# Performance work log

Measured on AMD Instinct MI355X. Metric: run time of the kernel, lower is better.

## Reference

```python
import jax, jax.numpy as jnp
from jax import lax
import numpy as np

B, N = 2, 261888          # images per GPU, total anchors (1024px FPN)
PRE_NMS = 6000            # config.PRE_NMS_LIMIT
PROPOSAL_COUNT = 1000     # proposal_count
NMS_THR = 0.7             # nms_threshold
STD = jnp.array([0.1, 0.1, 0.2, 0.2], jnp.float32)  # RPN_BBOX_STD_DEV


def setup_inputs() -> dict:
    key = jax.random.key(0)
    k1, k2, k3, k4 = jax.random.split(key, 4)
    rpn_class = jax.random.uniform(k1, (B, N, 2), dtype=jnp.float32)
    rpn_bbox = jax.random.normal(k2, (B, N, 4), dtype=jnp.float32)
    # valid normalized anchors: y1x1 in [0,0.9], h/w in [0.01,0.11]
    yx1 = jax.random.uniform(k3, (B, N, 2), dtype=jnp.float32) * 0.9
    hw = jax.random.uniform(k4, (B, N, 2), dtype=jnp.float32) * 0.1 + 0.01
    anchors = jnp.concatenate([yx1, yx1 + hw], axis=-1)
    return {"rpn_class": rpn_class, "rpn_bbox": rpn_bbox, "anchors": anchors}


def apply_box_deltas(boxes, deltas):
    h = boxes[..., 2] - boxes[..., 0]
    w = boxes[..., 3] - boxes[..., 1]
    cy = boxes[..., 0] + 0.5 * h + deltas[..., 0] * h
    cx = boxes[..., 1] + 0.5 * w + deltas[..., 1] * w
    h = h * jnp.exp(deltas[..., 2])
    w = w * jnp.exp(deltas[..., 3])
    y1 = cy - 0.5 * h
    x1 = cx - 0.5 * w
    return jnp.stack([y1, x1, y1 + h, x1 + w], axis=-1)


def pairwise_iou(b):  # b: [K,4] (y1,x1,y2,x2)
    y1, x1, y2, x2 = b[:, 0], b[:, 1], b[:, 2], b[:, 3]
    area = (y2 - y1) * (x2 - x1)
    ih = jnp.maximum(jnp.minimum(y2[:, None], y2[None, :]) - jnp.maximum(y1[:, None], y1[None, :]), 0.0)
    iw = jnp.maximum(jnp.minimum(x2[:, None], x2[None, :]) - jnp.maximum(x1[:, None], x1[None, :]), 0.0)
    inter = ih * iw
    return inter / (area[:, None] + area[None, :] - inter + 1e-8)


def nms_single(boxes, scores):
    # boxes [K,4] already sorted by descending score (top_k sorted=True)
    K = boxes.shape[0]
    iou = pairwise_iou(boxes)  # [K,K]

    def step(keep, xs):
        i, row = xs
        kept = jnp.logical_not(jnp.any(keep & (row > NMS_THR)))
        return keep.at[i].set(kept), None

    keep, _ = lax.scan(step, jnp.zeros((K,), jnp.bool_), (jnp.arange(K), iou))
    masked = jnp.where(keep, scores, -jnp.inf)
    _, idx = lax.top_k(masked, PROPOSAL_COUNT)
    props = boxes[idx]                      # [P,4]
    valid = keep[idx][:, None]              # pad with zeros like tf NMS padding
    return jnp.where(valid, props, 0.0)


def reference(rpn_class, rpn_bbox, anchors):
    scores = rpn_class[:, :, 1]                       # [B,N]
    deltas = rpn_bbox * STD.reshape(1, 1, 4)          # [B,N,4]
    k = min(PRE_NMS, anchors.shape[1])
    _, ix = lax.top_k(scores, k)                      # [B,k] sorted desc
    scores_k = jnp.take_along_axis(scores, ix, axis=1)
    deltas_k = jnp.take_along_axis(deltas, ix[..., None], axis=1)
    anchors_k = jnp.take_along_axis(anchors, ix[..., None], axis=1)
    boxes = apply_box_deltas(anchors_k, deltas_k)
    boxes = jnp.clip(boxes, 0.0, 1.0)                 # window [0,0,1,1]
    return jax.vmap(nms_single)(boxes, scores_k)      # [B,PROPOSAL_COUNT,4]
```

## Files before the change

kernel.cpp:

```cpp
#include <hip/hip_runtime.h>
#include <cstdint>

#define BATCH   2
#define NANCH   261888
#define PRE_NMS 6000
#define PROP    1000
#define SEG_CAP 8192
#define ECAP    65536
#define NT      94
#define RG      2
#define NMS_THR 0.7f
#define FLOOR   63488
#define WIN     2048
#define CAND_CAP 16384

typedef unsigned long long u64;
typedef unsigned int u32;

#define META_OFF   0u
#define BOXES_OFF  256u
#define EDGES_OFF  262400u
#define HIST_OFF   786688u
#define RANK_OFF   803072u
#define SEG_OFF    819456u
#define CAND_OFF   950528u
#define ZERO_N     (2u * WIN)

__global__ void k_zero(u32* p, int n, int* meta) {
    int i = blockIdx.x * blockDim.x + threadIdx.x;
    if (i < n) p[i] = 0u;
    if (i < 8) meta[i] = 0;
}

__device__ __forceinline__ int score_bucket(float s) {
    int bk = (int)(s * 65536.0f);
    return bk < 0 ? 0 : (bk > 65535 ? 65535 : bk);
}

__global__ __launch_bounds__(256) void k_histcand(const float2* __restrict__ cls2,
                                                  int* __restrict__ hist,
                                                  int* __restrict__ meta,
                                                  u64* __restrict__ cand) {
    __shared__ u64 lbuf[512];
    __shared__ u32 lcnt;
    __shared__ int lbase;
    int b = blockIdx.y, t = threadIdx.x;
    if (t == 0) lcnt = 0;
    __syncthreads();
    int* ccnt = meta + 2;
    for (int i = blockIdx.x * 256 + t; i < NANCH; i += 256 * 256) {
        float s = cls2[(size_t)b * NANCH + i].y;
        int bk = score_bucket(s);
        if (bk >= FLOOR) {
            atomicAdd(&hist[b * WIN + (bk - FLOOR)], 1);
            u64 key = ((u64)__float_as_uint(s) << 32) | (u32)(~(u32)i);
            u32 lp = atomicAdd(&lcnt, 1u);
            if (lp < 512) lbuf[lp] = key;
            else {
                int gp = atomicAdd(&ccnt[b], 1);
                if (gp < CAND_CAP) cand[b * CAND_CAP + gp] = key;
            }
        }
    }
    __syncthreads();
    int n = lcnt < 512u ? (int)lcnt : 512;
    if (t == 0) lbase = n ? atomicAdd(&ccnt[b], n) : 0;
    __syncthreads();
    for (int k = t; k < n; k += 256) {
        int gp = lbase + k;
        if (gp < CAND_CAP) cand[b * CAND_CAP + gp] = lbuf[k];
    }
}

__global__ __launch_bounds__(256) void k_ranks(const int* __restrict__ hist,
                                               int* __restrict__ rank_start,
                                               int* __restrict__ meta) {
    __shared__ int s[256];
    int b = blockIdx.x, t = threadIdx.x;
    const int* h = hist + b * WIN;
    int base = t * 8;
    int hv[8];
    int sum = 0;
    for (int c = 0; c < 8; ++c) { hv[c] = h[base + c]; sum += hv[c]; }
    s[t] = sum;
    __syncthreads();
    for (int off = 1; off < 256; off <<= 1) {
        int add = (t + off < 256) ? s[t + off] : 0;
        __syncthreads();
        s[t] += add;
        __syncthreads();
    }
    int above = (t + 1 < 256) ? s[t + 1] : 0;
    int acc = 0;
    int* rs = rank_start + b * WIN;
    for (int c = 7; c >= 0; --c) {
        int r = above + acc;
        rs[base + c] = r;
        acc += hv[c];
        if (r < PRE_NMS && r + hv[c] >= PRE_NMS) meta[b] = FLOOR + base + c;
    }
    if (t == 0 && s[0] < PRE_NMS) meta[b] = FLOOR;
}

__global__ __launch_bounds__(256) void k_scatterbuild(const u64* __restrict__ cand,
                                                      const int* __restrict__ meta,
                                                      int* __restrict__ rank,
                                                      u64* __restrict__ seg,
                                                      const float4* __restrict__ anchors,
                                                      const float4* __restrict__ bbox,
                                                      float4* __restrict__ boxes) {
    #pragma clang fp contract(off)
    int b = blockIdx.y;
    int thr = meta[b];
    int cc = meta[2 + b]; if (cc > CAND_CAP) cc = CAND_CAP;
    int idx = blockIdx.x * 256 + threadIdx.x;
    if (idx >= cc) return;
    u64 key = cand[b * CAND_CAP + idx];
    float s = __uint_as_float((u32)(key >> 32));
    int bk = score_bucket(s);
    if (bk < thr) return;
    int slot = atomicAdd(&rank[b * WIN + (bk - FLOOR)], 1);
    if (slot >= SEG_CAP) return;
    seg[(b << 13) + slot] = key;
    u32 ai = ~(u32)(key & 0xffffffffull);
    float4 a = anchors[(size_t)b * NANCH + ai];
    float4 d = bbox[(size_t)b * NANCH + ai];
    float dy = d.x * 0.1f, dx = d.y * 0.1f, dh = d.z * 0.2f, dw = d.w * 0.2f;
    float h = a.z - a.x;
    float w = a.w - a.y;
    float cy = a.x + 0.5f * h + dy * h;
    float cx = a.y + 0.5f * w + dx * w;
    h = h * expf(dh);
    w = w * expf(dw);
    float y1 = cy - 0.5f * h;
    float x1 = cx - 0.5f * w;
    float y2 = y1 + h;
    float x2 = x1 + w;
    y1 = fminf(fmaxf(y1, 0.f), 1.f);
    x1 = fminf(fmaxf(x1, 0.f), 1.f);
    y2 = fminf(fmaxf(y2, 0.f), 1.f);
    x2 = fminf(fmaxf(x2, 0.f), 1.f);
    boxes[(b << 13) + slot] = make_float4(y1, x1, y2, x2);
}

__global__ __launch_bounds__(256) void k_bsort(const int* __restrict__ meta,
                                               const int* __restrict__ rank,
                                               u64* __restrict__ seg,
                                               float4* __restrict__ boxes) {
    int b = blockIdx.y;
    int bkw = blockIdx.x * 256 + threadIdx.x;
    if (FLOOR + bkw < meta[b]) return;
    int en = rank[b * WIN + bkw]; if (en > SEG_CAP) en = SEG_CAP;
    int st = (bkw + 1 < WIN) ? rank[b * WIN + bkw + 1] : 0;
    if (st >= en - 1) return;
    u64* sg = seg + (b << 13);
    float4* bx = boxes + (b << 13);
    for (int i = st; i < en - 1; ++i) {
        u64 best = sg[i]; int bi = i;
        for (int j = i + 1; j < en; ++j) {
            u64 v = sg[j];
            if (v > best) { best = v; bi = j; }
        }
        if (bi != i) {
            sg[bi] = sg[i]; sg[i] = best;
            float4 tmp = bx[bi]; bx[bi] = bx[i]; bx[i] = tmp;
        }
    }
}

__global__ __launch_bounds__(256) void k_mask(const float4* __restrict__ boxes,
                                              u32* __restrict__ edges, int* __restrict__ ecnt) {
    #pragma clang fp contract(off)
    __shared__ float4 tb[64];
    __shared__ float ta69[64];
    int gx = blockIdx.x, T = blockIdx.y, b = blockIdx.z;
    if (gx * 8 + 7 < T) return;
    int wv = threadIdx.x >> 6, lane = threadIdx.x & 63;
    if (threadIdx.x < 64) {
        int c = T * 64 + threadIdx.x;
        float4 v = (c < PRE_NMS) ? boxes[(b << 13) + c] : make_float4(0.f, 0.f, 0.f, 0.f);
        tb[threadIdx.x] = v;
        ta69[threadIdx.x] = 0.69f * ((v.z - v.x) * (v.w - v.y));
    }
    __syncthreads();
    int W0 = gx * 8 + wv * RG;
    if (W0 + RG - 1 < T) return;
    float4 rb[RG]; float a69[RG]; float area_r[RG]; int jg[RG];
    #pragma unroll
    for (int r = 0; r < RG; ++r) {
        int W = W0 + r;
        int j = W * 64 + lane;
        bool ok = (W < NT) && (j < PRE_NMS);
        float4 v = ok ? boxes[(b << 13) + j] : make_float4(0.f, 0.f, 0.f, 0.f);
        rb[r] = v;
        float ar = (v.z - v.x) * (v.w - v.y);
        area_r[r] = ar;
        a69[r] = 0.69f * ar;
        jg[r] = j;
    }
    for (int c = 0; c < 64; ++c) {
        float4 bi = tb[c];
        float t69 = ta69[c];
        int ig = T * 64 + c;
        #pragma unroll
        for (int r = 0; r < RG; ++r) {
            float ih = fminf(bi.z, rb[r].z) - fmaxf(bi.x, rb[r].x); ih = fmaxf(ih, 0.f);
            float iw = fminf(bi.w, rb[r].w) - fmaxf(bi.y, rb[r].y); iw = fmaxf(iw, 0.f);
            float inter = ih * iw;
            if (inter > fmaxf(t69, a69[r])) {
                float ai = (bi.z - bi.x) * (bi.w - bi.y);
                float iou = inter / (ai + area_r[r] - inter + 1e-8f);
                if (iou > NMS_THR && ig < jg[r]) {
                    int pos = atomicAdd(&ecnt[b], 1);
                    if (pos < ECAP) edges[(b << 16) + pos] = ((u32)jg[r] << 13) | (u32)ig;
                }
            }
        }
    }
}

__global__ __launch_bounds__(512) void k_resolveout(const u32* __restrict__ edges,
                                                    const int* __restrict__ ecnt,
                                                    const float4* __restrict__ boxes,
                                                    float* __restrict__ out) {
    __shared__ unsigned char st[6016];
    __shared__ u32 cnt[6016];
    __shared__ u64 kw[NT];
    __shared__ int wp[NT + 1];
    __shared__ int changed;
    int b = blockIdx.x, t = threadIdx.x;
    int E = ecnt[b]; if (E > ECAP) E = ECAP;
    const u32* eb = edges + ((size_t)b << 16);
    for (int i = t; i < PROP * 4; i += 512) out[b * PROP * 4 + i] = 0.f;
    for (int j = t; j < 6016; j += 512) st[j] = 1;
    __syncthreads();
    for (int k = t; k < E; k += 512) st[eb[k] >> 13] = 0;
    __syncthreads();
    while (true) {
        if (t == 0) changed = 0;
        __syncthreads();
        for (int k = t; k < E; k += 512) {
            u32 e = eb[k]; int i = e & 8191, j = e >> 13;
            if (st[i] == 1 && st[j] == 0) { st[j] = 2; changed = 1; }
        }
        __syncthreads();
        for (int j = t; j < 6016; j += 512) cnt[j] = 0;
        __syncthreads();
        for (int k = t; k < E; k += 512) {
            u32 e = eb[k]; int i = e & 8191, j = e >> 13;
            if (st[i] != 2) atomicAdd(&cnt[j], 1u);
        }
        __syncthreads();
        for (int j = t; j < 6016; j += 512) {
            if (st[j] == 0 && cnt[j] == 0) { st[j] = 1; changed = 1; }
        }
        __syncthreads();
        if (!changed) break;
    }
    if (t < NT) {
        int base = t * 64;
        int lim = PRE_NMS - base; if (lim > 64) lim = 64;
        u64 bits = 0;
        for (int l = 0; l < lim; ++l) if (st[base + l] == 1) bits |= (1ull << l);
        kw[t] = bits;
        wp[t + 1] = __popcll(bits);
    }
    if (t == 0) wp[0] = 0;
    __syncthreads();
    if (t == 0) { for (int i = 1; i <= NT; ++i) wp[i] += wp[i - 1]; }
    __syncthreads();
    float4* out4 = (float4*)(out + b * PROP * 4);
    for (int j = t; j < PRE_NMS; j += 512) {
        u64 w = kw[j >> 6];
        int bit = j & 63;
        if ((w >> bit) & 1ull) {
            int rank = wp[j >> 6] + __popcll(w & ((1ull << bit) - 1ull));
            if (rank < PROP) out4[rank] = boxes[(b << 13) + j];
        }
    }
}

extern "C" void kernel_launch(void* const* d_in, const int* in_sizes, int n_in,
                              void* d_out, int out_size, void* d_ws, size_t ws_size,
                              hipStream_t stream) {
    const float2* cls2    = (const float2*)d_in[0];
    const float4* bbox    = (const float4*)d_in[1];
    const float4* anchors = (const float4*)d_in[2];
    float* out = (float*)d_out;
    char* w = (char*)d_ws;
    int*    meta   = (int*)(w + META_OFF);
    float4* boxes  = (float4*)(w + BOXES_OFF);
    u32*    edges  = (u32*)(w + EDGES_OFF);
    int*    hist   = (int*)(w + HIST_OFF);
    int*    rank   = (int*)(w + RANK_OFF);
    u64*    seg    = (u64*)(w + SEG_OFF);
    u64*    cand   = (u64*)(w + CAND_OFF);

    k_zero<<<dim3((ZERO_N + 255) / 256), 256, 0, stream>>>((u32*)hist, ZERO_N, meta);
    k_histcand<<<dim3(256, BATCH), 256, 0, stream>>>(cls2, hist, meta, cand);
    k_ranks<<<dim3(BATCH), 256, 0, stream>>>(hist, rank, meta);
    k_scatterbuild<<<dim3(CAND_CAP / 256, BATCH), 256, 0, stream>>>(cand, meta, rank, seg,
                                                                    anchors, bbox, boxes);
    k_bsort<<<dim3(WIN / 256, BATCH), 256, 0, stream>>>(meta, rank, seg, boxes);
    k_mask<<<dim3((NT + 7) / 8, NT, BATCH), 256, 0, stream>>>(boxes, edges, meta + 4);
    k_resolveout<<<dim3(BATCH), 512, 0, stream>>>(edges, meta + 4, boxes, out);
}
```

Measured before the change: 129.9 us.

## Drop zero kernel and global histogram atomics; use per-block candidate segments

Removes the k_zero launch and the global histogram atomics. Each histcand block now writes its candidates to its own fixed segment along with a count, and k_ranks rebuilds the histogram in shared memory from those segments. The scatter kernel reads per-block segments with 64 threads, and the prefix sum in resolveout becomes a parallel scan instead of a serial loop. The trade-off is that k_ranks does the histogram serially in only two blocks, and candidates beyond 1024 per block are dropped.

New measurement: 125.7 us. -3.2%, faster.

```diff
diff --git a/kernel.cpp b/kernel.cpp
--- a/kernel.cpp
+++ b/kernel.cpp
@@ -12,7 +12,7 @@
 #define NMS_THR 0.7f
 #define FLOOR   63488
 #define WIN     2048
-#define CAND_CAP 16384
+#define BSEG    1024
 
 typedef unsigned long long u64;
 typedef unsigned int u32;
@@ -20,17 +20,10 @@
 #define META_OFF   0u
 #define BOXES_OFF  256u
 #define EDGES_OFF  262400u
-#define HIST_OFF   786688u
-#define RANK_OFF   803072u
-#define SEG_OFF    819456u
-#define CAND_OFF   950528u
-#define ZERO_N     (2u * WIN)
-
-__global__ void k_zero(u32* p, int n, int* meta) {
-    int i = blockIdx.x * blockDim.x + threadIdx.x;
-    if (i < n) p[i] = 0u;
-    if (i < 8) meta[i] = 0;
-}
+#define RANK_OFF   786688u
+#define SEG_OFF    803072u
+#define BCNT_OFF   934144u
+#define CAND_OFF   936192u
 
 __device__ __forceinline__ int score_bucket(float s) {
     int bk = (int)(s * 65536.0f);
@@ -38,50 +31,49 @@
 }
 
 __global__ __launch_bounds__(256) void k_histcand(const float2* __restrict__ cls2,
-                                                  int* __restrict__ hist,
-                                                  int* __restrict__ meta,
+                                                  int* __restrict__ bcnt,
                                                   u64* __restrict__ cand) {
-    __shared__ u64 lbuf[512];
+    __shared__ u64 lbuf[BSEG];
     __shared__ u32 lcnt;
-    __shared__ int lbase;
-    int b = blockIdx.y, t = threadIdx.x;
+    int b = blockIdx.y, blk = blockIdx.x, t = threadIdx.x;
     if (t == 0) lcnt = 0;
     __syncthreads();
-    int* ccnt = meta + 2;
-    for (int i = blockIdx.x * 256 + t; i < NANCH; i += 256 * 256) {
+    for (int i = blk * 256 + t; i < NANCH; i += 256 * 256) {
         float s = cls2[(size_t)b * NANCH + i].y;
         int bk = score_bucket(s);
         if (bk >= FLOOR) {
-            atomicAdd(&hist[b * WIN + (bk - FLOOR)], 1);
             u64 key = ((u64)__float_as_uint(s) << 32) | (u32)(~(u32)i);
             u32 lp = atomicAdd(&lcnt, 1u);
-            if (lp < 512) lbuf[lp] = key;
-            else {
-                int gp = atomicAdd(&ccnt[b], 1);
-                if (gp < CAND_CAP) cand[b * CAND_CAP + gp] = key;
-            }
-        }
-    }
-    __syncthreads();
-    int n = lcnt < 512u ? (int)lcnt : 512;
-    if (t == 0) lbase = n ? atomicAdd(&ccnt[b], n) : 0;
-    __syncthreads();
-    for (int k = t; k < n; k += 256) {
-        int gp = lbase + k;
-        if (gp < CAND_CAP) cand[b * CAND_CAP + gp] = lbuf[k];
-    }
-}
-
-__global__ __launch_bounds__(256) void k_ranks(const int* __restrict__ hist,
+            if (lp < BSEG) lbuf[lp] = key;
+        }
+    }
+    __syncthreads();
+    int n = lcnt < (u32)BSEG ? (int)lcnt : BSEG;
+    if (t == 0) bcnt[b * 256 + blk] = n;
+    u64* dst = cand + ((size_t)(b * 256 + blk) << 10);
+    for (int k = t; k < n; k += 256) dst[k] = lbuf[k];
+}
+
+__global__ __launch_bounds__(256) void k_ranks(const int* __restrict__ bcnt,
+                                               const u64* __restrict__ cand,
                                                int* __restrict__ rank_start,
                                                int* __restrict__ meta) {
+    __shared__ int hist[WIN];
     __shared__ int s[256];
     int b = blockIdx.x, t = threadIdx.x;
-    const int* h = hist + b * WIN;
+    for (int c = t; c < WIN; c += 256) hist[c] = 0;
+    __syncthreads();
+    int cnt = bcnt[b * 256 + t];
+    const u64* src = cand + ((size_t)(b * 256 + t) << 10);
+    for (int k = 0; k < cnt; ++k) {
+        float sc = __uint_as_float((u32)(src[k] >> 32));
+        atomicAdd(&hist[score_bucket(sc) - FLOOR], 1);
+    }
+    __syncthreads();
     int base = t * 8;
     int hv[8];
     int sum = 0;
-    for (int c = 0; c < 8; ++c) { hv[c] = h[base + c]; sum += hv[c]; }
+    for (int c = 0; c < 8; ++c) { hv[c] = hist[base + c]; sum += hv[c]; }
     s[t] = sum;
     __syncthreads();
     for (int off = 1; off < 256; off <<= 1) {
@@ -99,48 +91,53 @@
         acc += hv[c];
         if (r < PRE_NMS && r + hv[c] >= PRE_NMS) meta[b] = FLOOR + base + c;
     }
-    if (t == 0 && s[0] < PRE_NMS) meta[b] = FLOOR;
-}
-
-__global__ __launch_bounds__(256) void k_scatterbuild(const u64* __restrict__ cand,
-                                                      const int* __restrict__ meta,
-                                                      int* __restrict__ rank,
-                                                      u64* __restrict__ seg,
-                                                      const float4* __restrict__ anchors,
-                                                      const float4* __restrict__ bbox,
-                                                      float4* __restrict__ boxes) {
+    if (t == 0) {
+        meta[4 + b] = 0;
+        if (s[0] < PRE_NMS) meta[b] = FLOOR;
+    }
+}
+
+__global__ __launch_bounds__(64) void k_scatterbuild(const u64* __restrict__ cand,
+                                                     const int* __restrict__ bcnt,
+                                                     const int* __restrict__ meta,
+                                                     int* __restrict__ rank,
+                                                     u64* __restrict__ seg,
+                                                     const float4* __restrict__ anchors,
+                                                     const float4* __restrict__ bbox,
+                                                     float4* __restrict__ boxes) {
     #pragma clang fp contract(off)
-    int b = blockIdx.y;
+    int b = blockIdx.y, blk = blockIdx.x;
     int thr = meta[b];
-    int cc = meta[2 + b]; if (cc > CAND_CAP) cc = CAND_CAP;
-    int idx = blockIdx.x * 256 + threadIdx.x;
-    if (idx >= cc) return;
-    u64 key = cand[b * CAND_CAP + idx];
-    float s = __uint_as_float((u32)(key >> 32));
-    int bk = score_bucket(s);
-    if (bk < thr) return;
-    int slot = atomicAdd(&rank[b * WIN + (bk - FLOOR)], 1);
-    if (slot >= SEG_CAP) return;
-    seg[(b << 13) + slot] = key;
-    u32 ai = ~(u32)(key & 0xffffffffull);
-    float4 a = anchors[(size_t)b * NANCH + ai];
-    float4 d = bbox[(size_t)b * NANCH + ai];
-    float dy = d.x * 0.1f, dx = d.y * 0.1f, dh = d.z * 0.2f, dw = d.w * 0.2f;
-    float h = a.z - a.x;
-    float w = a.w - a.y;
-    float cy = a.x + 0.5f * h + dy * h;
-    float cx = a.y + 0.5f * w + dx * w;
-    h = h * expf(dh);
-    w = w * expf(dw);
-    float y1 = cy - 0.5f * h;
-    float x1 = cx - 0.5f * w;
-    float y2 = y1 + h;
-    float x2 = x1 + w;
-    y1 = fminf(fmaxf(y1, 0.f), 1.f);
-    x1 = fminf(fmaxf(x1, 0.f), 1.f);
-    y2 = fminf(fmaxf(y2, 0.f), 1.f);
-    x2 = fminf(fmaxf(x2, 0.f), 1.f);
-    boxes[(b << 13) + slot] = make_float4(y1, x1, y2, x2);
+    int cc = bcnt[b * 256 + blk];
+    const u64* src = cand + ((size_t)(b * 256 + blk) << 10);
+    for (int idx = threadIdx.x; idx < cc; idx += 64) {
+        u64 key = src[idx];
+        float s = __uint_as_float((u32)(key >> 32));
+        int bk = score_bucket(s);
+        if (bk < thr) continue;
+        int slot = atomicAdd(&rank[b * WIN + (bk - FLOOR)], 1);
+        if (slot >= SEG_CAP) continue;
+        seg[(b << 13) + slot] = key;
+        u32 ai = ~(u32)(key & 0xffffffffull);
+        float4 a = anchors[(size_t)b * NANCH + ai];
+        float4 d = bbox[(size_t)b * NANCH + ai];
+        float dy = d.x * 0.1f, dx = d.y * 0.1f, dh = d.z * 0.2f, dw = d.w * 0.2f;
+        float h = a.z - a.x;
+        float w = a.w - a.y;
+        float cy = a.x + 0.5f * h + dy * h;
+        float cx = a.y + 0.5f * w + dx * w;
+        h = h * expf(dh);
+        w = w * expf(dw);
+        float y1 = cy - 0.5f * h;
+        float x1 = cx - 0.5f * w;
+        float y2 = y1 + h;
+        float x2 = x1 + w;
+        y1 = fminf(fmaxf(y1, 0.f), 1.f);
+        x1 = fminf(fmaxf(x1, 0.f), 1.f);
+        y2 = fminf(fmaxf(y2, 0.f), 1.f);
+        x2 = fminf(fmaxf(x2, 0.f), 1.f);
+        boxes[(b << 13) + slot] = make_float4(y1, x1, y2, x2);
+    }
 }
 
 __global__ __launch_bounds__(256) void k_bsort(const int* __restrict__ meta,
@@ -267,8 +264,13 @@
     }
     if (t == 0) wp[0] = 0;
     __syncthreads();
-    if (t == 0) { for (int i = 1; i <= NT; ++i) wp[i] += wp[i - 1]; }
-    __syncthreads();
+    #pragma unroll
+    for (int off = 1; off < 128; off <<= 1) {
+        int add = (t >= off && t <= NT) ? wp[t - off] : 0;
+        __syncthreads();
+        if (t <= NT) wp[t] += add;
+        __syncthreads();
+    }
     float4* out4 = (float4*)(out + b * PROP * 4);
     for (int j = t; j < PRE_NMS; j += 512) {
         u64 w = kw[j >> 6];
@@ -291,16 +293,15 @@
     int*    meta   = (int*)(w + META_OFF);
     float4* boxes  = (float4*)(w + BOXES_OFF);
     u32*    edges  = (u32*)(w + EDGES_OFF);
-    int*    hist   = (int*)(w + HIST_OFF);
     int*    rank   = (int*)(w + RANK_OFF);
     u64*    seg    = (u64*)(w + SEG_OFF);
+    int*    bcnt   = (int*)(w + BCNT_OFF);
     u64*    cand   = (u64*)(w + CAND_OFF);
 
-    k_zero<<<dim3((ZERO_N + 255) / 256), 256, 0, stream>>>((u32*)hist, ZERO_N, meta);
-    k_histcand<<<dim3(256, BATCH), 256, 0, stream>>>(cls2, hist, meta, cand);
-    k_ranks<<<dim3(BATCH), 256, 0, stream>>>(hist, rank, meta);
-    k_scatterbuild<<<dim3(CAND_CAP / 256, BATCH), 256, 0, stream>>>(cand, meta, rank, seg,
-                                                                    anchors, bbox, boxes);
+    k_histcand<<<dim3(256, BATCH), 256, 0, stream>>>(cls2, bcnt, cand);
+    k_ranks<<<dim3(BATCH), 256, 0, stream>>>(bcnt, cand, rank, meta);
+    k_scatterbuild<<<dim3(256, BATCH), 64, 0, stream>>>(cand, bcnt, meta, rank, seg,
+                                                        anchors, bbox, boxes);
     k_bsort<<<dim3(WIN / 256, BATCH), 256, 0, stream>>>(meta, rank, seg, boxes);
     k_mask<<<dim3((NT + 7) / 8, NT, BATCH), 256, 0, stream>>>(boxes, edges, meta + 4);
     k_resolveout<<<dim3(BATCH), 512, 0, stream>>>(edges, meta + 4, boxes, out);
```
